# Performance work log

Hardware: AMD Instinct MI355X
Metric: run time of the kernel (lower is better)

The kernel has to match this reference:

```python
import jax, jax.numpy as jnp
import numpy as np

EMBED_DIM = 768
N_HEADS = 12
TIME_RATIO = 0.5
HEAD_DIM = EMBED_DIM // N_HEADS          # 64
T_HEAD = int(HEAD_DIM * TIME_RATIO)      # 32 time dims per head
T_DIM = T_HEAD * N_HEADS                 # 384 time dims overall
EPS = 1e-5


def _ln(v, g, b):
    m = jnp.mean(v, axis=-1, keepdims=True)
    var = jnp.mean((v - m) ** 2, axis=-1, keepdims=True)
    return (v - m) * jax.lax.rsqrt(var + EPS) * g + b


def minkowski_ln(x, g_t, b_t, g_s, b_s):
    # normalize time-like and space-like channel groups separately
    xt, xs = x[..., :T_DIM], x[..., T_DIM:]
    return jnp.concatenate([_ln(xt, g_t, b_t), _ln(xs, g_s, b_s)], axis=-1)


def lorentz_attention(x, Wq, bq, Wk, bk, Wv, bv, Wo, bo):
    B, S, D = x.shape
    def heads(W, b):
        return (x @ W + b).reshape(B, S, N_HEADS, HEAD_DIM).transpose(0, 2, 1, 3)
    q, k, v = heads(Wq, bq), heads(Wk, bk), heads(Wv, bv)
    # Minkowski metric signature (-,...,-,+,...,+) within each head
    eta = jnp.concatenate([-jnp.ones((T_HEAD,), x.dtype), jnp.ones((HEAD_DIM - T_HEAD,), x.dtype)])
    logits = jnp.einsum('bhqd,bhkd->bhqk', q * eta, k) / np.sqrt(HEAD_DIM).astype(np.float32)
    attn = jax.nn.softmax(logits, axis=-1)
    o = jnp.einsum('bhqk,bhkd->bhqd', attn, v)
    o = o.transpose(0, 2, 1, 3).reshape(B, S, D)
    return o @ Wo + bo


def setup_inputs() -> dict:
    key = jax.random.key(0)
    ks = jax.random.split(key, 16)
    D, H4 = EMBED_DIM, EMBED_DIM * 4
    s = 0.02
    inp = {
        'x': jax.random.normal(ks[0], (2, 2048, D), jnp.float32),
        'Wq': jax.random.normal(ks[1], (D, D), jnp.float32) * s, 'bq': jnp.zeros((D,), jnp.float32),
        'Wk': jax.random.normal(ks[2], (D, D), jnp.float32) * s, 'bk': jnp.zeros((D,), jnp.float32),
        'Wv': jax.random.normal(ks[3], (D, D), jnp.float32) * s, 'bv': jnp.zeros((D,), jnp.float32),
        'Wo': jax.random.normal(ks[4], (D, D), jnp.float32) * s, 'bo': jnp.zeros((D,), jnp.float32),
        'g1t': jnp.ones((T_DIM,), jnp.float32), 'b1t': jnp.zeros((T_DIM,), jnp.float32),
        'g1s': jnp.ones((D - T_DIM,), jnp.float32), 'b1s': jnp.zeros((D - T_DIM,), jnp.float32),
        'W1': jax.random.normal(ks[5], (D, H4), jnp.float32) * s, 'bb1': jnp.zeros((H4,), jnp.float32),
        'W2': jax.random.normal(ks[6], (H4, D), jnp.float32) * s, 'bb2': jnp.zeros((D,), jnp.float32),
        'g2t': jnp.ones((T_DIM,), jnp.float32), 'b2t': jnp.zeros((T_DIM,), jnp.float32),
        'g2s': jnp.ones((D - T_DIM,), jnp.float32), 'b2s': jnp.zeros((D - T_DIM,), jnp.float32),
    }
    return inp


def reference(x, Wq, bq, Wk, bk, Wv, bv, Wo, bo,
              g1t, b1t, g1s, b1s, W1, bb1, W2, bb2,
              g2t, b2t, g2s, b2s):
    a = lorentz_attention(x, Wq, bq, Wk, bk, Wv, bv, Wo, bo)
    x = minkowski_ln(x + a, g1t, b1t, g1s, b1s)
    h = jax.nn.gelu(x @ W1 + bb1) @ W2 + bb2
    x = minkowski_ln(x + h, g2t, b2t, g2s, b2s)
    return x
```

## Files before the change

### kernel.cpp

```cpp
#include <hip/hip_runtime.h>
#include <cstddef>
#include <cstdint>

#define D_EMB  768
#define NHEAD  12
#define HDIM   64
#define THEAD  32
#define SEQ    2048
#define BATCH  2
#define NROW   (BATCH*SEQ)
#define HID4   3072

typedef unsigned short u16;
typedef __bf16 bf16x8 __attribute__((ext_vector_type(8)));
typedef float  f32x4  __attribute__((ext_vector_type(4)));
typedef unsigned short u16x8 __attribute__((ext_vector_type(8)));

__device__ __forceinline__ u16 f2bf(float f) {
    unsigned u = __builtin_bit_cast(unsigned, f);
    return (u16)((u + 0x7FFFu + ((u >> 16) & 1u)) >> 16);
}
__device__ __forceinline__ float bf2f(u16 h) {
    return __builtin_bit_cast(float, (unsigned)h << 16);
}
__device__ __forceinline__ u16 cvt_bf(float f) {
    return __builtin_bit_cast(u16, (__bf16)f);
}

__device__ __forceinline__ void gload_lds16(const void* g, void* l) {
    __builtin_amdgcn_global_load_lds(
        reinterpret_cast<const __attribute__((address_space(1))) void*>(
            reinterpret_cast<uintptr_t>(g)),
        reinterpret_cast<__attribute__((address_space(3))) void*>(
            (uint32_t)reinterpret_cast<uintptr_t>(l)),
        16, 0, 0);
}

__device__ __forceinline__ void tcast(float (*t)[33], const float* __restrict__ W,
                                      u16* __restrict__ WT, int K, int M,
                                      int mt, int kt)
{
    const int m0 = mt * 32, k0 = kt * 32;
    const int tx = threadIdx.x & 31, ty = threadIdx.x >> 5;
#pragma unroll
    for (int i = 0; i < 32; i += 8)
        t[ty + i][tx] = W[(size_t)(k0 + ty + i) * M + m0 + tx];
    __syncthreads();
#pragma unroll
    for (int i = 0; i < 32; i += 8)
        WT[(size_t)(m0 + ty + i) * K + k0 + tx] = f2bf(t[tx][ty + i]);
}

__global__ __launch_bounds__(256)
void prep(const float* __restrict__ Wq, const float* __restrict__ Wk,
          const float* __restrict__ Wv, const float* __restrict__ Wo,
          const float* __restrict__ W1, const float* __restrict__ W2,
          const float* __restrict__ bq, const float* __restrict__ bk,
          const float* __restrict__ bv, const float* __restrict__ x,
          u16* __restrict__ WqkvoT, u16* __restrict__ W1T,
          u16* __restrict__ W2T, u16* __restrict__ xb,
          float* __restrict__ bqkv)
{
    __shared__ float t[32][33];
    const int bid = blockIdx.x;
    if (bid < 2304) {
        const int z = bid / 576, r = bid % 576;
        const float* W = z == 0 ? Wq : z == 1 ? Wk : z == 2 ? Wv : Wo;
        tcast(t, W, WqkvoT + (size_t)z * 768 * 768, 768, 768, r % 24, r / 24);
    } else if (bid < 4608) {
        const int r = bid - 2304;
        tcast(t, W1, W1T, 768, 3072, r % 96, r / 96);
    } else if (bid < 6912) {
        const int r = bid - 4608;
        tcast(t, W2, W2T, 3072, 768, r % 24, r / 24);
    } else if (bid < 8448) {
        const int i = (bid - 6912) * 2048 + threadIdx.x * 8;
        const float4 a = *reinterpret_cast<const float4*>(x + i);
        const float4 b = *reinterpret_cast<const float4*>(x + i + 4);
        u16x8 h;
        h[0] = f2bf(a.x); h[1] = f2bf(a.y); h[2] = f2bf(a.z); h[3] = f2bf(a.w);
        h[4] = f2bf(b.x); h[5] = f2bf(b.y); h[6] = f2bf(b.z); h[7] = f2bf(b.w);
        *reinterpret_cast<u16x8*>(xb + i) = h;
    } else {
        const int i = (bid - 8448) * 256 + threadIdx.x;
        if (i < 2304)
            bqkv[i] = i < 768 ? bq[i] : (i < 1536 ? bk[i - 768] : bv[i - 1536]);
    }
}

template<int EPI>
__global__ __launch_bounds__(256)
void gemm_bf16(const u16* __restrict__ A, const u16* __restrict__ B,
               const float* __restrict__ bias, void* __restrict__ Cp,
               u16* __restrict__ VTp, int K, int N)
{
    __shared__ u16 As[2][128 * 32];
    __shared__ u16 Bs[2][128 * 32];
    const int tid  = threadIdx.x;
    const int lane = tid & 63;
    const int w    = tid >> 6;
    const int m0 = blockIdx.x * 128, n0 = blockIdx.y * 128;
    const int wr = (w >> 1) << 6, wc = (w & 1) << 6;

    const int seg0 = (w << 11) + lane * 16;
    const int row0 = seg0 >> 6, cb0 = (seg0 & 63) >> 1;
    const int seg1 = seg0 + 1024;
    const int row1 = seg1 >> 6, cb1 = (seg1 & 63) >> 1;
    const u16* a0 = A + (size_t)(m0 + row0) * K + cb0;
    const u16* a1 = A + (size_t)(m0 + row1) * K + cb1;
    const u16* b0 = B + (size_t)(n0 + row0) * K + cb0;
    const u16* b1 = B + (size_t)(n0 + row1) * K + cb1;
    const int lo0 = (w * 2 + 0) << 9;
    const int lo1 = (w * 2 + 1) << 9;

    int aIdx[4], bIdx[4];
#pragma unroll
    for (int i = 0; i < 4; ++i) {
        aIdx[i] = (wr + i * 16 + (lane & 15)) * 32 + ((lane >> 4) << 3);
        bIdx[i] = (wc + i * 16 + (lane & 15)) * 32 + ((lane >> 4) << 3);
    }

    f32x4 acc[4][4];
#pragma unroll
    for (int i = 0; i < 4; ++i)
#pragma unroll
        for (int j = 0; j < 4; ++j)
#pragma unroll
            for (int q = 0; q < 4; ++q) acc[i][j][q] = 0.f;

    gload_lds16(a0, &As[0][lo0]);
    gload_lds16(a1, &As[0][lo1]);
    gload_lds16(b0, &Bs[0][lo0]);
    gload_lds16(b1, &Bs[0][lo1]);
    __syncthreads();

    int cur = 0;
    for (int k0 = 0; k0 < K; k0 += 32) {
        if (k0 + 32 < K) {
            gload_lds16(a0 + k0 + 32, &As[cur ^ 1][lo0]);
            gload_lds16(a1 + k0 + 32, &As[cur ^ 1][lo1]);
            gload_lds16(b0 + k0 + 32, &Bs[cur ^ 1][lo0]);
            gload_lds16(b1 + k0 + 32, &Bs[cur ^ 1][lo1]);
        }
        bf16x8 af[4], bv[4];
#pragma unroll
        for (int i = 0; i < 4; ++i)
            af[i] = *reinterpret_cast<const bf16x8*>(&As[cur][aIdx[i]]);
#pragma unroll
        for (int j = 0; j < 4; ++j)
            bv[j] = *reinterpret_cast<const bf16x8*>(&Bs[cur][bIdx[j]]);
#pragma unroll
        for (int i = 0; i < 4; ++i)
#pragma unroll
            for (int j = 0; j < 4; ++j)
                acc[i][j] = __builtin_amdgcn_mfma_f32_16x16x32_bf16(
                    af[i], bv[j], acc[i][j], 0, 0, 0);
        __syncthreads();
        cur ^= 1;
    }

#pragma unroll
    for (int i = 0; i < 4; ++i) {
#pragma unroll
        for (int q = 0; q < 4; ++q) {
            const int row = m0 + wr + i * 16 + ((lane >> 4) << 2) + q;
#pragma unroll
            for (int j = 0; j < 4; ++j) {
                const int col = n0 + wc + j * 16 + (lane & 15);
                float v = acc[i][j][q] + bias[col];
                if (EPI == 2) {
                    const float z = 1.5957691216057308f *
                                    (v + 0.044715f * v * v * v);
                    const float e = __builtin_amdgcn_exp2f(z * -1.4426950408889634f);
                    v = v * __builtin_amdgcn_rcpf(1.f + e);
                    ((u16*)Cp)[(size_t)row * N + col] = cvt_bf(v);
                } else {
                    if (n0 < 1536) {
                        ((u16*)Cp)[(size_t)row * 1536 + col] = cvt_bf(v);
                    } else {
                        const int c2 = col - 1536;
                        const int hh = c2 >> 6, dd = c2 & 63;
                        const int bb = row >> 11, tok = row & 2047;
                        const int t = tok & 63;
                        const int p = ((t & 15) << 2) | (t >> 4);
                        VTp[((size_t)(bb * NHEAD + hh) * HDIM + dd) * SEQ
                            + (tok & ~63) + p] = cvt_bf(v);
                    }
                }
            }
        }
    }
}

__global__ __launch_bounds__(256)
void gemm_n64(const u16* __restrict__ A, const u16* __restrict__ B,
              const float* __restrict__ bias, u16* __restrict__ C0,
              u16* __restrict__ C1, int Khalf, int Ktot, int N)
{
    __shared__ u16 As[2][64 * 32];
    __shared__ u16 Bs[2][128 * 32];
    const int tid  = threadIdx.x;
    const int lane = tid & 63;
    const int w    = tid >> 6;
    const int l15  = lane & 15;
    const int g    = lane >> 4;
    const int m0 = blockIdx.x * 64, n0 = blockIdx.y * 128;
    const int zz = blockIdx.z;
    const int kbase = zz * Khalf;
    u16* __restrict__ C = zz ? C1 : C0;

    const int segA = (w << 10) + lane * 16;
    const int rowA = segA >> 6, cbA = (segA & 63) >> 1;
    const u16* aP = A + (size_t)(m0 + rowA) * Ktot + kbase + cbA;
    const int loA = w << 9;
    const int seg0 = (w << 11) + lane * 16;
    const int row0 = seg0 >> 6, cb0 = (seg0 & 63) >> 1;
    const int seg1 = seg0 + 1024;
    const int row1 = seg1 >> 6, cb1 = (seg1 & 63) >> 1;
    const u16* b0 = B + (size_t)(n0 + row0) * Ktot + kbase + cb0;
    const u16* b1 = B + (size_t)(n0 + row1) * Ktot + kbase + cb1;
    const int lo0 = w << 10, lo1 = (w << 10) + 512;

    int aIdx[4], bIdx[2];
#pragma unroll
    for (int i = 0; i < 4; ++i) aIdx[i] = (i * 16 + l15) * 32 + (g << 3);
#pragma unroll
    for (int j = 0; j < 2; ++j) bIdx[j] = ((w << 5) + j * 16 + l15) * 32 + (g << 3);

    f32x4 acc[4][2];
#pragma unroll
    for (int i = 0; i < 4; ++i)
#pragma unroll
        for (int j = 0; j < 2; ++j)
#pragma unroll
            for (int q = 0; q < 4; ++q) acc[i][j][q] = 0.f;

    gload_lds16(aP, &As[0][loA]);
    gload_lds16(b0, &Bs[0][lo0]);
    gload_lds16(b1, &Bs[0][lo1]);
    __syncthreads();

    int cur = 0;
    for (int k0 = 0; k0 < Khalf; k0 += 32) {
        if (k0 + 32 < Khalf) {
            gload_lds16(aP + k0 + 32, &As[cur ^ 1][loA]);
            gload_lds16(b0 + k0 + 32, &Bs[cur ^ 1][lo0]);
            gload_lds16(b1 + k0 + 32, &Bs[cur ^ 1][lo1]);
        }
        bf16x8 af[4], bv[2];
#pragma unroll
        for (int i = 0; i < 4; ++i)
            af[i] = *reinterpret_cast<const bf16x8*>(&As[cur][aIdx[i]]);
#pragma unroll
        for (int j = 0; j < 2; ++j)
            bv[j] = *reinterpret_cast<const bf16x8*>(&Bs[cur][bIdx[j]]);
#pragma unroll
        for (int i = 0; i < 4; ++i)
#pragma unroll
            for (int j = 0; j < 2; ++j)
                acc[i][j] = __builtin_amdgcn_mfma_f32_16x16x32_bf16(
                    af[i], bv[j], acc[i][j], 0, 0, 0);
        __syncthreads();
        cur ^= 1;
    }

#pragma unroll
    for (int i = 0; i < 4; ++i) {
#pragma unroll
        for (int q = 0; q < 4; ++q) {
            const int row = m0 + i * 16 + (g << 2) + q;
#pragma unroll
            for (int j = 0; j < 2; ++j) {
                const int col = n0 + (w << 5) + j * 16 + l15;
                const float bb = zz ? 0.f : bias[col];
                C[(size_t)row * N + col] = cvt_bf(acc[i][j][q] + bb);
            }
        }
    }
}

#define SM_SCALE 0.18033688011112042f

__global__ __launch_bounds__(256)
void attn_mfma(const u16* __restrict__ QK, const u16* __restrict__ VT,
               u16* __restrict__ O)
{
    __shared__ u16 Ks[2][64 * 64];
    __shared__ u16 Vs[2][64 * 64];
    __shared__ u16 Ps[64 * 72];

    const int tid  = threadIdx.x;
    const int lane = tid & 63;
    const int w    = tid >> 6;
    const int l15  = lane & 15;
    const int g    = lane >> 4;
    const int bh   = blockIdx.x;
    const int b    = bh / NHEAD, h = bh % NHEAD;
    const int q0   = blockIdx.y * 64;
    const int bS   = b * SEQ;

    bf16x8 aq[2];
    {
        const u16* Qg = QK + (size_t)(bS + q0 + (w << 4) + l15) * 1536 + h * HDIM;
#pragma unroll
        for (int kk = 0; kk < 2; ++kk) {
            const u16x8 hq = *reinterpret_cast<const u16x8*>(Qg + kk * 32 + g * 8);
            const float sc = (kk == 0) ? -SM_SCALE : SM_SCALE;
            u16x8 hs;
#pragma unroll
            for (int j = 0; j < 8; ++j)
                hs[j] = cvt_bf(bf2f(hq[j]) * sc);
            aq[kk] = __builtin_bit_cast(bf16x8, hs);
        }
    }

    const int rl = lane >> 3;
    const int cs = ((lane & 7) ^ rl) << 3;
    const u16* pK = QK + (size_t)(bS + 16 * w + rl) * 1536 + 768 + h * HDIM + cs;
    const u16* pV = VT + ((size_t)(b * NHEAD + h) * HDIM + 16 * w + rl) * SEQ + cs;

    int swz[2];
#pragma unroll
    for (int kk = 0; kk < 2; ++kk)
        swz[kk] = ((kk * 4 + g) ^ (l15 & 7)) << 3;

    bf16x8 vones;
    {
        u16x8 o16;
#pragma unroll
        for (int j = 0; j < 8; ++j) o16[j] = 0x3F80u;
        vones = __builtin_bit_cast(bf16x8, o16);
    }

    f32x4 accO[4];
#pragma unroll
    for (int n = 0; n < 4; ++n)
#pragma unroll
        for (int q = 0; q < 4; ++q) accO[n][q] = 0.f;
    f32x4 accS;
#pragma unroll
    for (int q = 0; q < 4; ++q) accS[q] = 0.f;

#define ATTN_STAGE(c, kt)                                                   \
    do {                                                                    \
        u16* dK = &Ks[c][w * 1024];                                         \
        u16* dV = &Vs[c][w * 1024];                                         \
        gload_lds16(pK + (size_t)(kt) * 1536,       dK);                    \
        gload_lds16(pK + (size_t)((kt) + 8) * 1536, dK + 512);              \
        gload_lds16(pV + (kt),           dV);                               \
        gload_lds16(pV + (kt) + 8 * SEQ, dV + 512);                         \
    } while (0)

    ATTN_STAGE(0, 0);
    __syncthreads();
    int cur = 0;

    for (int kt = 0; kt < SEQ; kt += 64) {
        if (kt + 64 < SEQ) ATTN_STAGE(cur ^ 1, kt + 64);

        f32x4 sac[4];
        __builtin_amdgcn_s_setprio(1);
#pragma unroll
        for (int n = 0; n < 4; ++n) {
#pragma unroll
            for (int q = 0; q < 4; ++q) sac[n][q] = 0.f;
#pragma unroll
            for (int kk = 0; kk < 2; ++kk) {
                const bf16x8 bk = *reinterpret_cast<const bf16x8*>(
                    &Ks[cur][(n * 16 + l15) * 64 + swz[kk]]);
                sac[n] = __builtin_amdgcn_mfma_f32_16x16x32_bf16(
                    aq[kk], bk, sac[n], 0, 0, 0);
            }
        }
        __builtin_amdgcn_s_setprio(0);

#pragma unroll
        for (int r4 = 0; r4 < 4; ++r4) {
            const int prow = (w << 4) + (g << 2) + r4;
            const float sv0 = __builtin_amdgcn_exp2f(sac[0][r4]);
            const float sv1 = __builtin_amdgcn_exp2f(sac[1][r4]);
            const float sv2 = __builtin_amdgcn_exp2f(sac[2][r4]);
            const float sv3 = __builtin_amdgcn_exp2f(sac[3][r4]);
            ushort4 pk4;
            pk4.x = cvt_bf(sv0);
            pk4.y = cvt_bf(sv1);
            pk4.z = cvt_bf(sv2);
            pk4.w = cvt_bf(sv3);
            *reinterpret_cast<ushort4*>(&Ps[prow * 72 + (l15 << 2)]) = pk4;
        }

        bf16x8 pa[2];
#pragma unroll
        for (int kk = 0; kk < 2; ++kk)
            pa[kk] = *reinterpret_cast<const bf16x8*>(
                &Ps[((w << 4) + l15) * 72 + kk * 32 + g * 8]);
        __builtin_amdgcn_s_setprio(1);
#pragma unroll
        for (int n = 0; n < 4; ++n) {
#pragma unroll
            for (int kk = 0; kk < 2; ++kk) {
                const bf16x8 bv = *reinterpret_cast<const bf16x8*>(
                    &Vs[cur][(n * 16 + l15) * 64 + swz[kk]]);
                accO[n] = __builtin_amdgcn_mfma_f32_16x16x32_bf16(
                    pa[kk], bv, accO[n], 0, 0, 0);
            }
        }
#pragma unroll
        for (int kk = 0; kk < 2; ++kk)
            accS = __builtin_amdgcn_mfma_f32_16x16x32_bf16(
                pa[kk], vones, accS, 0, 0, 0);
        __builtin_amdgcn_s_setprio(0);
        __syncthreads();
        cur ^= 1;
    }

#pragma unroll
    for (int r4 = 0; r4 < 4; ++r4) {
        const float inv = 1.f / accS[r4];
        const int qr = q0 + (w << 4) + (g << 2) + r4;
#pragma unroll
        for (int n = 0; n < 4; ++n)
            O[(size_t)(bS + qr) * D_EMB + h * HDIM + n * 16 + l15]
                = cvt_bf(accO[n][r4] * inv);
    }
#undef ATTN_STAGE
}

template<int XBF>
__global__ __launch_bounds__(256)
void mink_ln(const void* __restrict__ Xp, const u16* __restrict__ R1,
             const u16* __restrict__ R2,
             const float* __restrict__ gt, const float* __restrict__ bt,
             const float* __restrict__ gs, const float* __restrict__ bs,
             float* __restrict__ Out, u16* __restrict__ OutB, int nrows)
{
    const int wid  = (int)((blockIdx.x * 256 + threadIdx.x) >> 6);
    const int lane = threadIdx.x & 63;
    const int row  = wid >> 1, half = wid & 1;
    if (row >= nrows) return;

    const float* g  = half ? gs : gt;
    const float* bb = half ? bs : bt;
    const size_t base = (size_t)row * D_EMB + half * 384;

    float v[6];
    float sum = 0.f;
#pragma unroll
    for (int i = 0; i < 3; ++i) {
        const size_t e = base + i * 128 + lane * 2;
        float x0, x1;
        if (XBF) {
            const unsigned xv = *reinterpret_cast<const unsigned*>(
                (const u16*)Xp + e);
            x0 = bf2f((u16)xv); x1 = bf2f((u16)(xv >> 16));
        } else {
            const float2 xf = *reinterpret_cast<const float2*>(
                (const float*)Xp + e);
            x0 = xf.x; x1 = xf.y;
        }
        const unsigned r1 = *reinterpret_cast<const unsigned*>(R1 + e);
        const unsigned r2 = *reinterpret_cast<const unsigned*>(R2 + e);
        const float t0 = x0 + bf2f((u16)r1) + bf2f((u16)r2);
        const float t1 = x1 + bf2f((u16)(r1 >> 16)) + bf2f((u16)(r2 >> 16));
        v[2 * i] = t0; v[2 * i + 1] = t1;
        sum += t0 + t1;
    }
#pragma unroll
    for (int off = 32; off; off >>= 1) sum += __shfl_xor(sum, off);
    const float mean = sum * (1.f / 384.f);

    float ss = 0.f;
#pragma unroll
    for (int i = 0; i < 6; ++i) { const float d = v[i] - mean; ss += d * d; }
#pragma unroll
    for (int off = 32; off; off >>= 1) ss += __shfl_xor(ss, off);
    const float rstd = rsqrtf(ss * (1.f / 384.f) + 1e-5f);

#pragma unroll
    for (int i = 0; i < 3; ++i) {
        const int e = i * 128 + lane * 2;
        const float o0 = (v[2 * i]     - mean) * rstd * g[e]     + bb[e];
        const float o1 = (v[2 * i + 1] - mean) * rstd * g[e + 1] + bb[e + 1];
        if (Out) {
            float2 of; of.x = o0; of.y = o1;
            *reinterpret_cast<float2*>(Out + base + e) = of;
        }
        if (OutB) {
            const unsigned pk = (unsigned)cvt_bf(o0) |
                                ((unsigned)cvt_bf(o1) << 16);
            *reinterpret_cast<unsigned*>(OutB + base + e) = pk;
        }
    }
}

extern "C" void kernel_launch(void* const* d_in, const int* in_sizes, int n_in,
                              void* d_out, int out_size, void* d_ws, size_t ws_size,
                              hipStream_t stream)
{
    const float* x   = (const float*)d_in[0];
    const float* Wq  = (const float*)d_in[1];
    const float* bq  = (const float*)d_in[2];
    const float* Wk  = (const float*)d_in[3];
    const float* bk  = (const float*)d_in[4];
    const float* Wv  = (const float*)d_in[5];
    const float* bv  = (const float*)d_in[6];
    const float* Wo  = (const float*)d_in[7];
    const float* bo  = (const float*)d_in[8];
    const float* g1t = (const float*)d_in[9];
    const float* b1t = (const float*)d_in[10];
    const float* g1s = (const float*)d_in[11];
    const float* b1s = (const float*)d_in[12];
    const float* W1  = (const float*)d_in[13];
    const float* bb1 = (const float*)d_in[14];
    const float* W2  = (const float*)d_in[15];
    const float* bb2 = (const float*)d_in[16];
    const float* g2t = (const float*)d_in[17];
    const float* b2t = (const float*)d_in[18];
    const float* g2s = (const float*)d_in[19];
    const float* b2s = (const float*)d_in[20];
    float* out = (float*)d_out;

    const size_t ND = (size_t)NROW * D_EMB;
    u16* WqkvoT = (u16*)d_ws;
    u16* W1T = WqkvoT + 2359296;
    u16* W2T = W1T + 2359296;
    u16* xb  = W2T + 2359296;
    u16* QKb = xb + ND;
    u16* VTb = QKb + (size_t)NROW * 1536;
    u16* Ab  = VTb + ND;
    u16* Hb  = QKb;
    float* bqkv = (float*)(Ab + ND);
    u16* AoFb = (u16*)(Ab + ND);
    u16* QKfb = (u16*)QKb;
    u16* X2b  = (u16*)((float*)(Ab + ND) + ND);

    const dim3 blk(256);

    prep<<<8457, blk, 0, stream>>>(Wq, Wk, Wv, Wo, W1, W2, bq, bk, bv, x,
                                   WqkvoT, W1T, W2T, xb, bqkv);

    gemm_bf16<3><<<dim3(32, 18), blk, 0, stream>>>(xb, WqkvoT, bqkv, QKb, VTb,
                                                   768, 2304);
    attn_mfma<<<dim3(BATCH * NHEAD, SEQ / 64), blk, 0, stream>>>(QKb, VTb, Ab);

    gemm_n64<<<dim3(64, 6, 2), blk, 0, stream>>>(
        Ab, WqkvoT + (size_t)2304 * 768, bo, AoFb, QKfb, 384, 768, 768);
    mink_ln<0><<<2048, blk, 0, stream>>>(x, AoFb, QKfb, g1t, b1t, g1s, b1s,
                                         nullptr, xb, NROW);
    gemm_bf16<2><<<dim3(32, 24), blk, 0, stream>>>(xb, W1T, bb1, Hb, nullptr,
                                                   768, 3072);
    gemm_n64<<<dim3(64, 6, 2), blk, 0, stream>>>(
        Hb, W2T, bb2, AoFb, X2b, 1536, 3072, 768);
    mink_ln<1><<<2048, blk, 0, stream>>>(xb, AoFb, X2b, g2t, b2t, g2s, b2s,
                                         out, nullptr, NROW);
}
```

Baseline: 177.6 us.

## Split attention keys across two blocks and double query rows per wave

Each attention block now handles 128 queries, two 16-row groups per wave, so every K/V tile staged in LDS feeds twice as many MFMAs. The key range is split in half across a new grid z dimension. Each half writes unnormalized bf16 partial outputs and float row sums, and a new attn_merge kernel adds the halves and normalizes them. The block count stays the same while global K/V traffic per query drops. The cost is an extra kernel launch, extra workspace read/write traffic, higher register pressure, and an added bf16 rounding of partial outputs.

```diff
diff --git a/kernel.cpp b/kernel.cpp
--- a/kernel.cpp
+++ b/kernel.cpp
@@ -283,11 +283,12 @@
 
 __global__ __launch_bounds__(256)
 void attn_mfma(const u16* __restrict__ QK, const u16* __restrict__ VT,
-               u16* __restrict__ O)
+               u16* __restrict__ O0, u16* __restrict__ O1,
+               float* __restrict__ Sp)
 {
     __shared__ u16 Ks[2][64 * 64];
     __shared__ u16 Vs[2][64 * 64];
-    __shared__ u16 Ps[64 * 72];
+    __shared__ u16 Ps[128 * 72];
 
     const int tid  = threadIdx.x;
     const int lane = tid & 63;
@@ -296,12 +297,16 @@
     const int g    = lane >> 4;
     const int bh   = blockIdx.x;
     const int b    = bh / NHEAD, h = bh % NHEAD;
-    const int q0   = blockIdx.y * 64;
+    const int q0   = blockIdx.y * 128;
+    const int z    = blockIdx.z;
+    const int keybase = z * 1024;
     const int bS   = b * SEQ;
 
-    bf16x8 aq[2];
-    {
-        const u16* Qg = QK + (size_t)(bS + q0 + (w << 4) + l15) * 1536 + h * HDIM;
+    bf16x8 aq[2][2];
+#pragma unroll
+    for (int qb = 0; qb < 2; ++qb) {
+        const u16* Qg = QK + (size_t)(bS + q0 + w * 32 + qb * 16 + l15) * 1536
+                        + h * HDIM;
 #pragma unroll
         for (int kk = 0; kk < 2; ++kk) {
             const u16x8 hq = *reinterpret_cast<const u16x8*>(Qg + kk * 32 + g * 8);
@@ -310,14 +315,16 @@
 #pragma unroll
             for (int j = 0; j < 8; ++j)
                 hs[j] = cvt_bf(bf2f(hq[j]) * sc);
-            aq[kk] = __builtin_bit_cast(bf16x8, hs);
+            aq[qb][kk] = __builtin_bit_cast(bf16x8, hs);
         }
     }
 
     const int rl = lane >> 3;
     const int cs = ((lane & 7) ^ rl) << 3;
-    const u16* pK = QK + (size_t)(bS + 16 * w + rl) * 1536 + 768 + h * HDIM + cs;
-    const u16* pV = VT + ((size_t)(b * NHEAD + h) * HDIM + 16 * w + rl) * SEQ + cs;
+    const u16* pK = QK + (size_t)(bS + keybase + 16 * w + rl) * 1536
+                    + 768 + h * HDIM + cs;
+    const u16* pV = VT + ((size_t)(b * NHEAD + h) * HDIM + 16 * w + rl) * SEQ
+                    + keybase + cs;
 
     int swz[2];
 #pragma unroll
@@ -332,14 +339,18 @@
         vones = __builtin_bit_cast(bf16x8, o16);
     }
 
-    f32x4 accO[4];
-#pragma unroll
-    for (int n = 0; n < 4; ++n)
-#pragma unroll
-        for (int q = 0; q < 4; ++q) accO[n][q] = 0.f;
-    f32x4 accS;
-#pragma unroll
-    for (int q = 0; q < 4; ++q) accS[q] = 0.f;
+    f32x4 accO[2][4];
+#pragma unroll
+    for (int qb = 0; qb < 2; ++qb)
+#pragma unroll
+        for (int n = 0; n < 4; ++n)
+#pragma unroll
+            for (int q = 0; q < 4; ++q) accO[qb][n][q] = 0.f;
+    f32x4 accS[2];
+#pragma unroll
+    for (int qb = 0; qb < 2; ++qb)
+#pragma unroll
+        for (int q = 0; q < 4; ++q) accS[qb][q] = 0.f;
 
 #define ATTN_STAGE(c, kt)                                                   \
     do {                                                                    \
@@ -355,45 +366,54 @@
     __syncthreads();
     int cur = 0;
 
-    for (int kt = 0; kt < SEQ; kt += 64) {
-        if (kt + 64 < SEQ) ATTN_STAGE(cur ^ 1, kt + 64);
-
-        f32x4 sac[4];
+    for (int kt = 0; kt < 1024; kt += 64) {
+        if (kt + 64 < 1024) ATTN_STAGE(cur ^ 1, kt + 64);
+
+        f32x4 sac[2][4];
         __builtin_amdgcn_s_setprio(1);
 #pragma unroll
         for (int n = 0; n < 4; ++n) {
-#pragma unroll
-            for (int q = 0; q < 4; ++q) sac[n][q] = 0.f;
 #pragma unroll
             for (int kk = 0; kk < 2; ++kk) {
                 const bf16x8 bk = *reinterpret_cast<const bf16x8*>(
                     &Ks[cur][(n * 16 + l15) * 64 + swz[kk]]);
-                sac[n] = __builtin_amdgcn_mfma_f32_16x16x32_bf16(
-                    aq[kk], bk, sac[n], 0, 0, 0);
+#pragma unroll
+                for (int qb = 0; qb < 2; ++qb) {
+                    if (kk == 0) {
+#pragma unroll
+                        for (int q = 0; q < 4; ++q) sac[qb][n][q] = 0.f;
+                    }
+                    sac[qb][n] = __builtin_amdgcn_mfma_f32_16x16x32_bf16(
+                        aq[qb][kk], bk, sac[qb][n], 0, 0, 0);
+                }
             }
         }
         __builtin_amdgcn_s_setprio(0);
 
 #pragma unroll
-        for (int r4 = 0; r4 < 4; ++r4) {
-            const int prow = (w << 4) + (g << 2) + r4;
-            const float sv0 = __builtin_amdgcn_exp2f(sac[0][r4]);
-            const float sv1 = __builtin_amdgcn_exp2f(sac[1][r4]);
-            const float sv2 = __builtin_amdgcn_exp2f(sac[2][r4]);
-            const float sv3 = __builtin_amdgcn_exp2f(sac[3][r4]);
-            ushort4 pk4;
-            pk4.x = cvt_bf(sv0);
-            pk4.y = cvt_bf(sv1);
-            pk4.z = cvt_bf(sv2);
-            pk4.w = cvt_bf(sv3);
-            *reinterpret_cast<ushort4*>(&Ps[prow * 72 + (l15 << 2)]) = pk4;
-        }
-
-        bf16x8 pa[2];
-#pragma unroll
-        for (int kk = 0; kk < 2; ++kk)
-            pa[kk] = *reinterpret_cast<const bf16x8*>(
-                &Ps[((w << 4) + l15) * 72 + kk * 32 + g * 8]);
+        for (int qb = 0; qb < 2; ++qb)
+#pragma unroll
+            for (int r4 = 0; r4 < 4; ++r4) {
+                const int prow = w * 32 + qb * 16 + (g << 2) + r4;
+                const float sv0 = __builtin_amdgcn_exp2f(sac[qb][0][r4]);
+                const float sv1 = __builtin_amdgcn_exp2f(sac[qb][1][r4]);
+                const float sv2 = __builtin_amdgcn_exp2f(sac[qb][2][r4]);
+                const float sv3 = __builtin_amdgcn_exp2f(sac[qb][3][r4]);
+                ushort4 pk4;
+                pk4.x = cvt_bf(sv0);
+                pk4.y = cvt_bf(sv1);
+                pk4.z = cvt_bf(sv2);
+                pk4.w = cvt_bf(sv3);
+                *reinterpret_cast<ushort4*>(&Ps[prow * 72 + (l15 << 2)]) = pk4;
+            }
+
+        bf16x8 pa[2][2];
+#pragma unroll
+        for (int qb = 0; qb < 2; ++qb)
+#pragma unroll
+            for (int kk = 0; kk < 2; ++kk)
+                pa[qb][kk] = *reinterpret_cast<const bf16x8*>(
+                    &Ps[(w * 32 + qb * 16 + l15) * 72 + kk * 32 + g * 8]);
         __builtin_amdgcn_s_setprio(1);
 #pragma unroll
         for (int n = 0; n < 4; ++n) {
@@ -401,29 +421,60 @@
             for (int kk = 0; kk < 2; ++kk) {
                 const bf16x8 bv = *reinterpret_cast<const bf16x8*>(
                     &Vs[cur][(n * 16 + l15) * 64 + swz[kk]]);
-                accO[n] = __builtin_amdgcn_mfma_f32_16x16x32_bf16(
-                    pa[kk], bv, accO[n], 0, 0, 0);
+#pragma unroll
+                for (int qb = 0; qb < 2; ++qb)
+                    accO[qb][n] = __builtin_amdgcn_mfma_f32_16x16x32_bf16(
+                        pa[qb][kk], bv, accO[qb][n], 0, 0, 0);
             }
         }
 #pragma unroll
-        for (int kk = 0; kk < 2; ++kk)
-            accS = __builtin_amdgcn_mfma_f32_16x16x32_bf16(
-                pa[kk], vones, accS, 0, 0, 0);
+        for (int qb = 0; qb < 2; ++qb)
+#pragma unroll
+            for (int kk = 0; kk < 2; ++kk)
+                accS[qb] = __builtin_amdgcn_mfma_f32_16x16x32_bf16(
+                    pa[qb][kk], vones, accS[qb], 0, 0, 0);
         __builtin_amdgcn_s_setprio(0);
         __syncthreads();
         cur ^= 1;
     }
 
-#pragma unroll
-    for (int r4 = 0; r4 < 4; ++r4) {
-        const float inv = 1.f / accS[r4];
-        const int qr = q0 + (w << 4) + (g << 2) + r4;
-#pragma unroll
-        for (int n = 0; n < 4; ++n)
-            O[(size_t)(bS + qr) * D_EMB + h * HDIM + n * 16 + l15]
-                = cvt_bf(accO[n][r4] * inv);
-    }
+    u16* __restrict__ Oz = z ? O1 : O0;
+#pragma unroll
+    for (int qb = 0; qb < 2; ++qb)
+#pragma unroll
+        for (int r4 = 0; r4 < 4; ++r4) {
+            const int qr = q0 + w * 32 + qb * 16 + (g << 2) + r4;
+#pragma unroll
+            for (int n = 0; n < 4; ++n)
+                Oz[(size_t)(bS + qr) * D_EMB + h * HDIM + n * 16 + l15]
+                    = cvt_bf(accO[qb][n][r4]);
+            if (l15 == 0)
+                Sp[(size_t)z * (BATCH * NHEAD * SEQ) + (b * NHEAD + h) * SEQ + qr]
+                    = accS[qb][r4];
+        }
 #undef ATTN_STAGE
+}
+
+__global__ __launch_bounds__(256)
+void attn_merge(const u16* __restrict__ O0, const u16* __restrict__ O1,
+                const float* __restrict__ Sp, u16* __restrict__ Ab)
+{
+    const int gid = blockIdx.x * 256 + threadIdx.x;
+    const size_t e = (size_t)gid * 8;
+    const int row = gid / 96;
+    const int cc  = gid % 96;
+    const int h   = cc >> 3;
+    const int b   = row >> 11, q = row & 2047;
+    const int si  = (b * NHEAD + h) * SEQ + q;
+    const float s = Sp[si] + Sp[(size_t)(BATCH * NHEAD * SEQ) + si];
+    const float inv = __builtin_amdgcn_rcpf(s);
+    const u16x8 a = *reinterpret_cast<const u16x8*>(O0 + e);
+    const u16x8 c = *reinterpret_cast<const u16x8*>(O1 + e);
+    u16x8 o;
+#pragma unroll
+    for (int j = 0; j < 8; ++j)
+        o[j] = cvt_bf((bf2f(a[j]) + bf2f(c[j])) * inv);
+    *reinterpret_cast<u16x8*>(Ab + e) = o;
 }
 
 template<int XBF>
@@ -530,9 +581,12 @@
     u16* Ab  = VTb + ND;
     u16* Hb  = QKb;
     float* bqkv = (float*)(Ab + ND);
-    u16* AoFb = (u16*)(Ab + ND);
+    u16* Op0 = (u16*)(Ab + ND);
+    u16* Op1 = Op0 + ND;
+    float* Sp = (float*)(Op1 + ND);
+    u16* AoFb = Op0;
     u16* QKfb = (u16*)QKb;
-    u16* X2b  = (u16*)((float*)(Ab + ND) + ND);
+    u16* X2b  = Op1;
 
     const dim3 blk(256);
 
@@ -541,7 +595,9 @@
 
     gemm_bf16<3><<<dim3(32, 18), blk, 0, stream>>>(xb, WqkvoT, bqkv, QKb, VTb,
                                                    768, 2304);
-    attn_mfma<<<dim3(BATCH * NHEAD, SEQ / 64), blk, 0, stream>>>(QKb, VTb, Ab);
+    attn_mfma<<<dim3(BATCH * NHEAD, SEQ / 128, 2), blk, 0, stream>>>(
+        QKb, VTb, Op0, Op1, Sp);
+    attn_merge<<<(int)(ND / 8 / 256), blk, 0, stream>>>(Op0, Op1, Sp, Ab);
 
     gemm_n64<<<dim3(64, 6, 2), blk, 0, stream>>>(
         Ab, WqkvoT + (size_t)2304 * 768, bo, AoFb, QKfb, 384, 768, 768);
```

Result: no change. 177.0 us (-0.3%).
